# Performance work log

Measured on AMD Instinct MI355X. Metric: run time of the kernel, lower is better.

## Reference

```python
import jax
jax.config.update("jax_enable_x64", True)  # codes use *1e12 factors; need int64
import jax.numpy as jnp
import numpy as np

# HashRectsPt hyperparameters (module buffers)
W0, H0 = 512.0, 512.0
ALPHA = 1.2
GAMMA = 0.6
BX, BY = 0.5, 0.5
N_RECTS = 8192


def setup_inputs() -> dict:
    key = jax.random.key(0)
    k1, k2, k3 = jax.random.split(key, 3)
    xy = jax.random.uniform(k1, (N_RECTS, 2), minval=0.0, maxval=2000.0)
    wh = jax.random.uniform(k2, (N_RECTS, 2), minval=8.0, maxval=512.0)
    rects = jnp.concatenate([xy, wh], axis=1).astype(jnp.float32)  # [N,4] x,y,w,h
    conf = jax.random.uniform(k3, (N_RECTS,), dtype=jnp.float32)
    return {"rects": rects, "conf": conf}


def _hash_codes(rects):
    # HashRectsPt.__call__ -> packed single int64 code per rect
    x, y, w, h = rects[:, 0], rects[:, 1], rects[:, 2], rects[:, 3]
    log_alpha = jnp.log(jnp.float32(ALPHA))
    i = jnp.round((jnp.log(jnp.float32(W0)) - jnp.log(w)) / log_alpha)
    j = jnp.round((jnp.log(jnp.float32(H0)) - jnp.log(h)) / log_alpha)
    gamma_ratio = (1.0 - GAMMA) / (1.0 + GAMMA)
    di = (W0 * gamma_ratio) / (ALPHA ** i)
    dj = (H0 * gamma_ratio) / (ALPHA ** j)
    # b_is_relative=True branch
    qx = jnp.round(x / di - BX)
    qy = jnp.round(y / dj - BY)
    codes = (qx.astype(jnp.int64)
             + qy.astype(jnp.int64) * 10_000
             + i.astype(jnp.int64) * 100_000_000
             + j.astype(jnp.int64) * 1_000_000_000_000)
    return codes  # [N] int64


def reference(rects, conf):
    codes = _hash_codes(rects)                         # [N]
    n = codes.shape[0]
    # torch.unique with data-dependent U -> padded fixed-size unique (U<=N);
    # pad value can never equal a real code, so padded columns match nothing.
    uniq = jnp.unique(codes, size=n, fill_value=jnp.iinfo(jnp.int64).min)  # [N]
    assign = codes[:, None] == uniq[None, :]           # [N, U] bool
    scores = conf[:, None] * assign.astype(conf.dtype)  # [N, U]
    # torch .max(dim=0) returns first max index; jnp.argmax matches.
    argidx = jnp.argmax(scores, axis=0)                # [U]
    return argidx
```

## Files before the change

### kernel.cpp

```cpp
#include <hip/hip_runtime.h>
#include <hip/hip_bf16.h>
#include <math.h>

#define N 8192
#define JS 64
#define SL (N / JS)
#define TPB 256
#define IT 4
#define IBT (TPB * IT)
#define NIB (N / IBT)

__device__ __forceinline__ unsigned pack_code(float x, float y, float w, float h) {
    const float LOG_ALPHA = (float)log((double)1.2f);
    const float LOGW0     = (float)log(512.0);
    float i_f = rintf((LOGW0 - (float)log((double)w)) / LOG_ALPHA);
    float j_f = rintf((LOGW0 - (float)log((double)h)) / LOG_ALPHA);
    float pi  = (float)pow((double)1.2f, (double)i_f);
    float pj  = (float)pow((double)1.2f, (double)j_f);
    float qx  = rintf(x / (128.0f / pi) - 0.5f);
    float qy  = rintf(y / (128.0f / pj) - 0.5f);
    return ((unsigned)(int)j_f << 27) | ((unsigned)(int)i_f << 22)
         | ((unsigned)(int)qy << 11) | (unsigned)(int)qx;
}

__global__ void k_codes(const float4* __restrict__ rects,
                        const float* __restrict__ conf,
                        unsigned* __restrict__ code32,
                        unsigned long long* __restrict__ pairw,
                        int* __restrict__ lose,
                        int* __restrict__ out) {
    int t = blockIdx.x * blockDim.x + threadIdx.x;
    float4 r = rects[t];
    unsigned c = pack_code(r.x, r.y, r.z, r.w);
    code32[t] = c;
    pairw[t]  = ((unsigned long long)c << 32) | (unsigned long long)__float_as_uint(conf[t]);
    lose[t] = 0;
    out[t]  = 0;
}

__global__ void __launch_bounds__(TPB)
k_winner(const unsigned long long* __restrict__ pairw, int* __restrict__ lose) {
    __shared__ unsigned long long s_w[SL];
    int t = threadIdx.x;
    int jb = blockIdx.y * SL;
    if (t < SL) s_w[t] = pairw[jb + t];

    int i0 = blockIdx.x * IBT + t;
    unsigned long long wi[IT], bd[IT];
    #pragma unroll
    for (int m = 0; m < IT; ++m) {
        wi[m] = pairw[i0 + m * TPB];
        bd[m] = (wi[m] | 0xFFFFFFFFULL) + 1ULL;
    }
    __syncthreads();

    int l[IT] = {0, 0, 0, 0};
    #pragma unroll 8
    for (int k = 0; k < SL; ++k) {
        unsigned long long wj = s_w[k];
        int jg = jb + k;
        #pragma unroll
        for (int m = 0; m < IT; ++m) {
            l[m] |= (int)(((wj > wi[m]) & (wj < bd[m])) |
                          ((wj == wi[m]) & (jg < i0 + m * TPB)));
        }
    }
    #pragma unroll
    for (int m = 0; m < IT; ++m)
        if (l[m]) atomicOr(&lose[i0 + m * TPB], 1);
}

__global__ void __launch_bounds__(TPB)
k_rank(const unsigned* __restrict__ code32, const int* __restrict__ lose,
       int* __restrict__ rank_part) {
    __shared__ unsigned s_v[SL];
    int t = threadIdx.x;
    int jb = blockIdx.y * SL;
    if (t < SL) s_v[t] = lose[jb + t] ? 0xFFFFFFFFu : code32[jb + t];

    int i0 = blockIdx.x * IBT + t;
    unsigned ci[IT];
    #pragma unroll
    for (int m = 0; m < IT; ++m) ci[m] = code32[i0 + m * TPB];
    __syncthreads();

    int r[IT] = {0, 0, 0, 0};
    #pragma unroll 8
    for (int k = 0; k < SL; ++k) {
        unsigned vj = s_v[k];
        #pragma unroll
        for (int m = 0; m < IT; ++m) r[m] += (int)(vj < ci[m]);
    }
    #pragma unroll
    for (int m = 0; m < IT; ++m)
        rank_part[blockIdx.y * N + i0 + m * TPB] = r[m];
}

__global__ void k_scatter(const float* __restrict__ conf,
                          const int* __restrict__ lose,
                          const int* __restrict__ rank_part,
                          int* __restrict__ out) {
    int i = blockIdx.x * blockDim.x + threadIdx.x;
    int r = 0;
    #pragma unroll
    for (int s = 0; s < JS; ++s) r += rank_part[s * N + i];
    if (lose[i] == 0) {
        out[r] = (conf[i] == 0.0f) ? 0 : i;
    }
}

extern "C" void kernel_launch(void* const* d_in, const int* in_sizes, int n_in,
                              void* d_out, int out_size, void* d_ws, size_t ws_size,
                              hipStream_t stream) {
    const float4* rects = (const float4*)d_in[0];
    const float*  conf  = (const float*)d_in[1];
    int* out = (int*)d_out;

    char* ws = (char*)d_ws;
    unsigned long long* pairw = (unsigned long long*)ws;
    unsigned* code32    = (unsigned*)(ws + N * 8);
    int*      lose      = (int*)(ws + N * 12);
    int*      rank_part = (int*)(ws + N * 16);

    k_codes  <<<N / 256, 256, 0, stream>>>(rects, conf, code32, pairw, lose, out);
    k_winner <<<dim3(NIB, JS), TPB, 0, stream>>>(pairw, lose);
    k_rank   <<<dim3(NIB, JS), TPB, 0, stream>>>(code32, lose, rank_part);
    k_scatter<<<N / 256, 256, 0, stream>>>(conf, lose, rank_part, out);
}
```

Before: 88.77 us.

## Fuse four kernels into one cooperative kernel with grid-wide syncs

```diff
diff --git a/kernel.cpp b/kernel.cpp
--- a/kernel.cpp
+++ b/kernel.cpp
@@ -1,14 +1,17 @@
 #include <hip/hip_runtime.h>
 #include <hip/hip_bf16.h>
+#include <hip/hip_cooperative_groups.h>
 #include <math.h>
 
+namespace cg = cooperative_groups;
+
 #define N 8192
+#define TPB 256
+#define BLKS 512
 #define JS 64
 #define SL (N / JS)
-#define TPB 256
 #define IT 4
 #define IBT (TPB * IT)
-#define NIB (N / IBT)
 
 __device__ __forceinline__ unsigned pack_code(float x, float y, float w, float h) {
     const float LOG_ALPHA = (float)log((double)1.2f);
@@ -23,89 +26,95 @@
          | ((unsigned)(int)qy << 11) | (unsigned)(int)qx;
 }
 
-__global__ void k_codes(const float4* __restrict__ rects,
-                        const float* __restrict__ conf,
-                        unsigned* __restrict__ code32,
-                        unsigned long long* __restrict__ pairw,
-                        int* __restrict__ lose,
-                        int* __restrict__ out) {
-    int t = blockIdx.x * blockDim.x + threadIdx.x;
-    float4 r = rects[t];
-    unsigned c = pack_code(r.x, r.y, r.z, r.w);
-    code32[t] = c;
-    pairw[t]  = ((unsigned long long)c << 32) | (unsigned long long)__float_as_uint(conf[t]);
-    lose[t] = 0;
-    out[t]  = 0;
-}
+__global__ void __launch_bounds__(TPB)
+k_all(const float4* __restrict__ rects, const float* __restrict__ conf,
+      unsigned* __restrict__ code32, unsigned long long* __restrict__ pairw,
+      int* __restrict__ flags, int* __restrict__ flag_part,
+      int* __restrict__ rank_part, int* __restrict__ out) {
+    cg::grid_group grid = cg::this_grid();
+    __shared__ unsigned long long s_w[SL];
+    const int b = blockIdx.x, t = threadIdx.x;
+    const int gid = b * TPB + t;
+    const int ib = b >> 6;
+    const int js = b & 63;
+    const int i0 = ib * IBT + t;
 
-__global__ void __launch_bounds__(TPB)
-k_winner(const unsigned long long* __restrict__ pairw, int* __restrict__ lose) {
-    __shared__ unsigned long long s_w[SL];
-    int t = threadIdx.x;
-    int jb = blockIdx.y * SL;
-    if (t < SL) s_w[t] = pairw[jb + t];
+    if (gid < N) {
+        float4 r = rects[gid];
+        unsigned c = pack_code(r.x, r.y, r.z, r.w);
+        code32[gid] = c;
+        pairw[gid]  = ((unsigned long long)c << 32)
+                    | (unsigned long long)__float_as_uint(conf[gid]);
+        out[gid] = 0;
+    }
+    grid.sync();
 
-    int i0 = blockIdx.x * IBT + t;
-    unsigned long long wi[IT], bd[IT];
-    #pragma unroll
-    for (int m = 0; m < IT; ++m) {
-        wi[m] = pairw[i0 + m * TPB];
-        bd[m] = (wi[m] | 0xFFFFFFFFULL) + 1ULL;
+    {
+        if (t < SL) s_w[t] = pairw[js * SL + t];
+        unsigned long long wi[IT];
+        #pragma unroll
+        for (int m = 0; m < IT; ++m) wi[m] = pairw[i0 + m * TPB];
+        __syncthreads();
+        int l[IT] = {0,0,0,0}, f[IT] = {0,0,0,0};
+        #pragma unroll 8
+        for (int k = 0; k < SL; ++k) {
+            unsigned long long wj = s_w[k];
+            int jg = js * SL + k;
+            #pragma unroll
+            for (int m = 0; m < IT; ++m) {
+                bool ceq = (unsigned)(wj >> 32) == (unsigned)(wi[m] >> 32);
+                bool g   = wj > wi[m];
+                bool e   = wj == wi[m];
+                bool d   = jg < i0 + m * TPB;
+                l[m] |= (int)(ceq & (g | (e & d)));
+                f[m] |= (int)(ceq & d);
+            }
+        }
+        #pragma unroll
+        for (int m = 0; m < IT; ++m)
+            flag_part[js * N + i0 + m * TPB] = l[m] | (f[m] << 1);
+        __syncthreads();
     }
-    __syncthreads();
+    grid.sync();
 
-    int l[IT] = {0, 0, 0, 0};
-    #pragma unroll 8
-    for (int k = 0; k < SL; ++k) {
-        unsigned long long wj = s_w[k];
-        int jg = jb + k;
+    if (gid < N) {
+        int fl = 0;
         #pragma unroll
-        for (int m = 0; m < IT; ++m) {
-            l[m] |= (int)(((wj > wi[m]) & (wj < bd[m])) |
-                          ((wj == wi[m]) & (jg < i0 + m * TPB)));
+        for (int s = 0; s < JS; ++s) fl |= flag_part[s * N + gid];
+        flags[gid] = fl;
+    }
+    grid.sync();
+
+    {
+        unsigned* s_v = (unsigned*)s_w;
+        if (t < SL) {
+            int j = js * SL + t;
+            s_v[t] = (flags[j] & 2) ? 0xFFFFFFFFu : code32[j];
         }
+        unsigned ci[IT];
+        #pragma unroll
+        for (int m = 0; m < IT; ++m) ci[m] = code32[i0 + m * TPB];
+        __syncthreads();
+        int r[IT] = {0,0,0,0};
+        #pragma unroll 8
+        for (int k = 0; k < SL; ++k) {
+            unsigned v = s_v[k];
+            #pragma unroll
+            for (int m = 0; m < IT; ++m) r[m] += (int)(v < ci[m]);
+        }
+        #pragma unroll
+        for (int m = 0; m < IT; ++m)
+            rank_part[js * N + i0 + m * TPB] = r[m];
     }
-    #pragma unroll
-    for (int m = 0; m < IT; ++m)
-        if (l[m]) atomicOr(&lose[i0 + m * TPB], 1);
-}
+    grid.sync();
 
-__global__ void __launch_bounds__(TPB)
-k_rank(const unsigned* __restrict__ code32, const int* __restrict__ lose,
-       int* __restrict__ rank_part) {
-    __shared__ unsigned s_v[SL];
-    int t = threadIdx.x;
-    int jb = blockIdx.y * SL;
-    if (t < SL) s_v[t] = lose[jb + t] ? 0xFFFFFFFFu : code32[jb + t];
-
-    int i0 = blockIdx.x * IBT + t;
-    unsigned ci[IT];
-    #pragma unroll
-    for (int m = 0; m < IT; ++m) ci[m] = code32[i0 + m * TPB];
-    __syncthreads();
-
-    int r[IT] = {0, 0, 0, 0};
-    #pragma unroll 8
-    for (int k = 0; k < SL; ++k) {
-        unsigned vj = s_v[k];
+    if (gid < N) {
+        int r = 0;
         #pragma unroll
-        for (int m = 0; m < IT; ++m) r[m] += (int)(vj < ci[m]);
-    }
-    #pragma unroll
-    for (int m = 0; m < IT; ++m)
-        rank_part[blockIdx.y * N + i0 + m * TPB] = r[m];
-}
-
-__global__ void k_scatter(const float* __restrict__ conf,
-                          const int* __restrict__ lose,
-                          const int* __restrict__ rank_part,
-                          int* __restrict__ out) {
-    int i = blockIdx.x * blockDim.x + threadIdx.x;
-    int r = 0;
-    #pragma unroll
-    for (int s = 0; s < JS; ++s) r += rank_part[s * N + i];
-    if (lose[i] == 0) {
-        out[r] = (conf[i] == 0.0f) ? 0 : i;
+        for (int s = 0; s < JS; ++s) r += rank_part[s * N + gid];
+        if (!(flags[gid] & 1)) {
+            out[r] = (conf[gid] == 0.0f) ? 0 : gid;
+        }
     }
 }
 
@@ -119,11 +128,12 @@
     char* ws = (char*)d_ws;
     unsigned long long* pairw = (unsigned long long*)ws;
     unsigned* code32    = (unsigned*)(ws + N * 8);
-    int*      lose      = (int*)(ws + N * 12);
-    int*      rank_part = (int*)(ws + N * 16);
+    int*      flags     = (int*)(ws + N * 12);
+    int*      flag_part = (int*)(ws + N * 16);
+    int*      rank_part = (int*)(ws + N * 16 + JS * N * 4);
 
-    k_codes  <<<N / 256, 256, 0, stream>>>(rects, conf, code32, pairw, lose, out);
-    k_winner <<<dim3(NIB, JS), TPB, 0, stream>>>(pairw, lose);
-    k_rank   <<<dim3(NIB, JS), TPB, 0, stream>>>(code32, lose, rank_part);
-    k_scatter<<<N / 256, 256, 0, stream>>>(conf, lose, rank_part, out);
+    void* args[] = { (void*)&rects, (void*)&conf, (void*)&code32, (void*)&pairw,
+                     (void*)&flags, (void*)&flag_part, (void*)&rank_part, (void*)&out };
+    hipLaunchCooperativeKernel((const void*)k_all, dim3(BLKS), dim3(TPB),
+                               args, 0, stream);
 }
```

Measured after the change: 298.5 us. 3.36x slower.
